# Optimization experiments

Measured on AMD Instinct MI355X. Metric: run time of the kernel, lower is better.

The kernel has to match this reference:

```python
import jax, jax.numpy as jnp
import numpy as np
import math

DIM = 2048
N_HEADS = 16
HEAD_DIM = DIM // N_HEADS
BASE = 10000
B, S = 2, 2048


def rope_cache(seq_len, head_dim, base):
    theta = 1.0 / (base ** (jnp.arange(0, head_dim, 2, dtype=jnp.float32)[: head_dim // 2] / head_dim))
    idx_theta = jnp.arange(seq_len, dtype=jnp.float32)[:, None] * theta[None, :]  # [S, D/2]
    return jnp.cos(idx_theta), jnp.sin(idx_theta)


def apply_rope(x, cos, sin):
    # x: [B, S, H, D]; cos/sin: [S, D/2]; interleaved-pair rotation
    b, s, h, d = x.shape
    xr = x.astype(jnp.float32).reshape(b, s, h, d // 2, 2)
    c = cos[None, :, None, :]
    sn = sin[None, :, None, :]
    x0, x1 = xr[..., 0], xr[..., 1]
    out = jnp.stack([x0 * c - x1 * sn, x1 * c + x0 * sn], axis=-1)
    return out.reshape(b, s, h, d).astype(x.dtype)


def setup_inputs() -> dict:
    key = jax.random.key(0)
    k1, k2, k3, k4, k5 = jax.random.split(key, 5)
    x = jax.random.normal(k1, (B, S, DIM), dtype=jnp.float32)
    # causal mask: True = masked out (strict upper triangle)
    mask = jnp.triu(jnp.ones((S, S), dtype=bool), k=1)[None, None]  # [1,1,S,S]
    scale = 0.02
    wq = jax.random.normal(k2, (DIM, DIM), dtype=jnp.float32) * scale
    wk = jax.random.normal(k3, (DIM, DIM), dtype=jnp.float32) * scale
    wv = jax.random.normal(k4, (DIM, DIM), dtype=jnp.float32) * scale
    wo = jax.random.normal(k5, (DIM, DIM), dtype=jnp.float32) * scale
    return {"x": x, "mask": mask, "wq": wq, "wk": wk, "wv": wv, "wo": wo}


def reference(x, mask, wq, wk, wv, wo):
    b, s, _ = x.shape
    cos, sin = rope_cache(s, HEAD_DIM, BASE)
    q = (x @ wq.T).reshape(b, s, N_HEADS, HEAD_DIM)
    k = (x @ wk.T).reshape(b, s, N_HEADS, HEAD_DIM)
    v = (x @ wv.T).reshape(b, s, N_HEADS, HEAD_DIM)
    q = apply_rope(q, cos, sin)
    k = apply_rope(k, cos, sin)
    # [B, H, S, S]
    scores = jnp.einsum('bqhd,bkhd->bhqk', q, k) / math.sqrt(HEAD_DIM)
    scores = jnp.where(mask, -jnp.inf, scores)
    attn = jax.nn.softmax(scores.astype(jnp.float32), axis=-1).astype(q.dtype)
    out = jnp.einsum('bhqk,bkhd->bqhd', attn, v).reshape(b, s, DIM)
    return out @ wo.T
```

## Files before the change

### kernel.cpp

```cpp
#include <hip/hip_runtime.h>
#include <hip/hip_bf16.h>
#include <math.h>

#define DIM   2048
#define NH    16
#define HD    128
#define SEQ   2048
#define BATCH 2
#define QKVN  6144

typedef __attribute__((ext_vector_type(8))) short short8;
typedef __attribute__((ext_vector_type(4))) float f32x4;
typedef __attribute__((ext_vector_type(4))) unsigned int u32x4;

static __device__ __forceinline__ unsigned short f2bf(float f) {
    __hip_bfloat16 h = __float2bfloat16(f);
    return *reinterpret_cast<unsigned short*>(&h);
}

static __device__ __forceinline__ void gload16(const __hip_bfloat16* g, __hip_bfloat16* l) {
    __builtin_amdgcn_global_load_lds(
        (__attribute__((address_space(1))) void*)(g),
        (__attribute__((address_space(3))) void*)(l), 16, 0, 0);
}

__global__ void cast_kernel(const float* __restrict__ in, __hip_bfloat16* __restrict__ out, int n) {
    int i = (blockIdx.x * blockDim.x + threadIdx.x) * 4;
    if (i >= n) return;
    float4 v = *(const float4*)(in + i);
    union { unsigned short u[4]; uint2 d; } pk;
    pk.u[0] = f2bf(v.x); pk.u[1] = f2bf(v.y); pk.u[2] = f2bf(v.z); pk.u[3] = f2bf(v.w);
    *(uint2*)(out + i) = pk.d;
}

__global__ void rope_kernel(__hip_bfloat16* __restrict__ qkv) {
    int idx = blockIdx.x * blockDim.x + threadIdx.x;
    int m    = idx >> 10;
    int rest = idx & 1023;
    int h    = rest >> 6;
    int i    = rest & 63;
    int s    = m & (SEQ - 1);
    float theta = __expf(-((float)(2 * i) * (1.0f / (float)HD)) * 9.210340371976184f);
    float ang = (float)s * theta;
    float sn, cs;
    sincosf(ang, &sn, &cs);
    size_t base = (size_t)m * QKVN + h * HD + 2 * i;
    float q0 = __bfloat162float(qkv[base]);
    float q1 = __bfloat162float(qkv[base + 1]);
    qkv[base]     = __float2bfloat16(q0 * cs - q1 * sn);
    qkv[base + 1] = __float2bfloat16(q1 * cs + q0 * sn);
    float k0 = __bfloat162float(qkv[base + DIM]);
    float k1 = __bfloat162float(qkv[base + DIM + 1]);
    qkv[base + DIM]     = __float2bfloat16(k0 * cs - k1 * sn);
    qkv[base + DIM + 1] = __float2bfloat16(k1 * cs + k0 * sn);
}

__global__ __launch_bounds__(256) void vtrans_kernel(const __hip_bfloat16* __restrict__ qkv,
                                                     __hip_bfloat16* __restrict__ vt) {
    __shared__ __align__(16) __hip_bfloat16 T[64 * 64];
    int tid = threadIdx.x;
    int s0 = blockIdx.x * 64;
    int d0 = blockIdx.y * 64;
    int b  = blockIdx.z;
#pragma unroll
    for (int i = 0; i < 2; i++) {
        int ch = tid + 256 * i;
        int r  = ch >> 3;
        int cc = ch & 7;
        u32x4 v = *(const u32x4*)(qkv + ((size_t)(b * SEQ + s0 + r)) * QKVN + 2 * DIM + d0 + cc * 8);
        __hip_bfloat16 tmp[8];
        *(u32x4*)tmp = v;
#pragma unroll
        for (int j = 0; j < 8; j++) {
            int dl = cc * 8 + j;
            int chunk = ((r >> 3) ^ (dl & 7) ^ (dl >> 3)) & 7;
            T[dl * 64 + chunk * 8 + (r & 7)] = tmp[j];
        }
    }
    __syncthreads();
#pragma unroll
    for (int i = 0; i < 2; i++) {
        int ch = tid + 256 * i;
        int dl = ch >> 3;
        int sc = ch & 7;
        int chunk = (sc ^ (dl & 7) ^ (dl >> 3)) & 7;
        u32x4 v = *(const u32x4*)(T + dl * 64 + chunk * 8);
        int d = d0 + dl;
        int h = d >> 7, dd = d & 127;
        *(u32x4*)(vt + ((size_t)((b * NH + h) * HD + dd)) * SEQ + s0 + sc * 8) = v;
    }
}

__device__ __forceinline__ void storeC(float* C, size_t idx, float v) { C[idx] = v; }
__device__ __forceinline__ void storeC(__hip_bfloat16* C, size_t idx, float v) { C[idx] = __float2bfloat16(v); }

template <typename OutT>
__global__ __launch_bounds__(256) void gemm_bt(const __hip_bfloat16* __restrict__ A,
                                               const __hip_bfloat16* __restrict__ B,
                                               OutT* __restrict__ C, int M, int N, int K) {
    constexpr int BK = 64;
    __shared__ __align__(16) __hip_bfloat16 As[128 * BK];
    __shared__ __align__(16) __hip_bfloat16 Bs[128 * BK];
    int tid  = threadIdx.x;
    int lane = tid & 63;
    int wave = tid >> 6;
    int quad = lane >> 4;
    int l15  = lane & 15;
    int wr   = wave >> 1, wc = wave & 1;
    int m0 = blockIdx.y * 128;
    int n0 = blockIdx.x * 128;
    f32x4 acc[4][4] = {};

    for (int k0 = 0; k0 < K; k0 += BK) {
        __syncthreads();
#pragma unroll
        for (int c = 0; c < 4; c++) {
            int br = (wave * 4 + c) * 8;
            int r  = br + (lane >> 3);
            int cc = (lane & 7) ^ (r & 7);
            gload16(A + (size_t)(m0 + r) * K + k0 + cc * 8, As + br * 64);
            gload16(B + (size_t)(n0 + r) * K + k0 + cc * 8, Bs + br * 64);
        }
        __syncthreads();
#pragma unroll
        for (int kk = 0; kk < BK; kk += 32) {
            short8 af[4], bf4[4];
#pragma unroll
            for (int t = 0; t < 4; t++) {
                int Ra = wr * 64 + t * 16 + l15;
                int pa = ((kk >> 3) + quad) ^ (Ra & 7);
                af[t] = *(const short8*)(As + Ra * 64 + pa * 8);
                int Rb = wc * 64 + t * 16 + l15;
                int pb = ((kk >> 3) + quad) ^ (Rb & 7);
                bf4[t] = *(const short8*)(Bs + Rb * 64 + pb * 8);
            }
#pragma unroll
            for (int mt = 0; mt < 4; mt++)
#pragma unroll
                for (int nt = 0; nt < 4; nt++)
                    acc[mt][nt] = __builtin_amdgcn_mfma_f32_16x16x32_bf16(af[mt], bf4[nt], acc[mt][nt], 0, 0, 0);
        }
    }
#pragma unroll
    for (int mt = 0; mt < 4; mt++)
#pragma unroll
        for (int nt = 0; nt < 4; nt++)
#pragma unroll
            for (int r = 0; r < 4; r++) {
                int row = m0 + wr * 64 + mt * 16 + quad * 4 + r;
                int col = n0 + wc * 64 + nt * 16 + l15;
                storeC(C, (size_t)row * N + col, acc[mt][nt][r]);
            }
}

__global__ __launch_bounds__(256) void flash_kernel(const __hip_bfloat16* __restrict__ qkv,
                                                    const __hip_bfloat16* __restrict__ vt,
                                                    __hip_bfloat16* __restrict__ attn) {
    __shared__ __align__(16) __hip_bfloat16 Ks[64 * 128];
    __shared__ __align__(16) __hip_bfloat16 Vts[128 * 64];
    constexpr int LDP = 72;
    __shared__ __align__(16) __hip_bfloat16 Ps[4 * 16 * LDP];
    int tid  = threadIdx.x;
    int lane = tid & 63;
    int wave = tid >> 6;
    int quad = lane >> 4;
    int l15  = lane & 15;
    int pairi = blockIdx.x;
    int bh = blockIdx.y;
    int b  = bh >> 4;
    int h  = bh & 15;
    size_t row0 = (size_t)b * SEQ;
    const __hip_bfloat16* vbase = vt + (size_t)bh * HD * SEQ;
    const float scale = 0.08838834764831845f;

    for (int seg = 0; seg < 2; seg++) {
        int qt = seg ? (31 - pairi) : pairi;
        short8 qf[4];
        {
            int qrow = qt * 64 + wave * 16 + l15;
            const __hip_bfloat16* qptr = qkv + (row0 + qrow) * (size_t)QKVN + h * HD + quad * 8;
#pragma unroll
            for (int c = 0; c < 4; c++) qf[c] = *(const short8*)(qptr + c * 32);
        }
        f32x4 o[8] = {};
        float mprev[4] = {-INFINITY, -INFINITY, -INFINITY, -INFINITY};
        float lsum[4]  = {0.f, 0.f, 0.f, 0.f};

        for (int kt = 0; kt <= qt; kt++) {
            __syncthreads();
#pragma unroll
            for (int c = 0; c < 4; c++) {
                int br = (wave * 4 + c) * 4;
                int r  = br + (lane >> 4);
                int cc = (lane & 15) ^ (r & 15);
                gload16(qkv + (row0 + kt * 64 + r) * (size_t)QKVN + DIM + h * HD + cc * 8,
                        Ks + br * 128);
            }
#pragma unroll
            for (int c = 0; c < 4; c++) {
                int br = (wave * 4 + c) * 8;
                int r  = br + (lane >> 3);
                int cc = (lane & 7) ^ (r & 7);
                gload16(vbase + (size_t)r * SEQ + kt * 64 + cc * 8, Vts + br * 64);
            }
            __syncthreads();

            f32x4 s[4];
#pragma unroll
            for (int nt = 0; nt < 4; nt++) {
                f32x4 a = {};
                int R = nt * 16 + l15;
#pragma unroll
                for (int c = 0; c < 4; c++) {
                    int phys = (c * 4 + quad) ^ (R & 15);
                    short8 kf = *(const short8*)(Ks + R * 128 + phys * 8);
                    a = __builtin_amdgcn_mfma_f32_16x16x32_bf16(qf[c], kf, a, 0, 0, 0);
                }
                s[nt] = a;
            }
            bool diag = (kt == qt);
#pragma unroll
            for (int nt = 0; nt < 4; nt++) {
                int key = kt * 64 + nt * 16 + l15;
#pragma unroll
                for (int r = 0; r < 4; r++) {
                    float v = s[nt][r] * scale;
                    if (diag) {
                        int q = qt * 64 + wave * 16 + quad * 4 + r;
                        if (key > q) v = -INFINITY;
                    }
                    s[nt][r] = v;
                }
            }
            float alpha[4];
#pragma unroll
            for (int r = 0; r < 4; r++) {
                float v = fmaxf(fmaxf(s[0][r], s[1][r]), fmaxf(s[2][r], s[3][r]));
                v = fmaxf(v, __shfl_xor(v, 1));
                v = fmaxf(v, __shfl_xor(v, 2));
                v = fmaxf(v, __shfl_xor(v, 4));
                v = fmaxf(v, __shfl_xor(v, 8));
                float mnew = fmaxf(mprev[r], v);
                alpha[r] = __expf(mprev[r] - mnew);
                mprev[r] = mnew;
            }
#pragma unroll
            for (int r = 0; r < 4; r++) {
                float sum = 0.f;
#pragma unroll
                for (int nt = 0; nt < 4; nt++) {
                    float p = __expf(s[nt][r] - mprev[r]);
                    s[nt][r] = p;
                    sum += p;
                }
                sum += __shfl_xor(sum, 1);
                sum += __shfl_xor(sum, 2);
                sum += __shfl_xor(sum, 4);
                sum += __shfl_xor(sum, 8);
                lsum[r] = lsum[r] * alpha[r] + sum;
            }
            __hip_bfloat16* pw = Ps + wave * 16 * LDP;
#pragma unroll
            for (int nt = 0; nt < 4; nt++)
#pragma unroll
                for (int r = 0; r < 4; r++)
                    pw[(quad * 4 + r) * LDP + nt * 16 + l15] = __float2bfloat16(s[nt][r]);
#pragma unroll
            for (int dt = 0; dt < 8; dt++)
#pragma unroll
                for (int r = 0; r < 4; r++) o[dt][r] *= alpha[r];
            short8 pf0 = *(const short8*)(pw + l15 * LDP + quad * 8);
            short8 pf1 = *(const short8*)(pw + l15 * LDP + 32 + quad * 8);
#pragma unroll
            for (int dt = 0; dt < 8; dt++) {
                int d = dt * 16 + l15;
                int p0 = (0 + quad) ^ (d & 7);
                int p1 = (4 + quad) ^ (d & 7);
                short8 vf0 = *(const short8*)(Vts + d * 64 + p0 * 8);
                short8 vf1 = *(const short8*)(Vts + d * 64 + p1 * 8);
                o[dt] = __builtin_amdgcn_mfma_f32_16x16x32_bf16(pf0, vf0, o[dt], 0, 0, 0);
                o[dt] = __builtin_amdgcn_mfma_f32_16x16x32_bf16(pf1, vf1, o[dt], 0, 0, 0);
            }
        }
        int qbase = qt * 64 + wave * 16 + quad * 4;
#pragma unroll
        for (int r = 0; r < 4; r++) {
            float inv = 1.0f / lsum[r];
#pragma unroll
            for (int dt = 0; dt < 8; dt++) {
                attn[(row0 + qbase + r) * (size_t)DIM + h * HD + dt * 16 + l15] =
                    __float2bfloat16(o[dt][r] * inv);
            }
        }
    }
}

extern "C" void kernel_launch(void* const* d_in, const int* in_sizes, int n_in,
                              void* d_out, int out_size, void* d_ws, size_t ws_size,
                              hipStream_t stream) {
    const float* x  = (const float*)d_in[0];
    const float* wq = (const float*)d_in[2];
    const float* wk = (const float*)d_in[3];
    const float* wv = (const float*)d_in[4];
    const float* wo = (const float*)d_in[5];
    float* out = (float*)d_out;

    char* ws = (char*)d_ws;
    __hip_bfloat16* xb    = (__hip_bfloat16*)(ws);
    __hip_bfloat16* attn  = (__hip_bfloat16*)(ws);
    __hip_bfloat16* wqkvb = (__hip_bfloat16*)(ws + 16777216ull);
    __hip_bfloat16* wob   = (__hip_bfloat16*)(ws + 41943040ull);
    __hip_bfloat16* qkv   = (__hip_bfloat16*)(ws + 50331648ull);
    __hip_bfloat16* vtg   = (__hip_bfloat16*)(ws + 100663296ull);

    const int nx = BATCH * SEQ * DIM;
    const int nw = DIM * DIM;
    cast_kernel<<<nx / 4 / 256, 256, 0, stream>>>(x, xb, nx);
    cast_kernel<<<nw / 4 / 256, 256, 0, stream>>>(wq, wqkvb, nw);
    cast_kernel<<<nw / 4 / 256, 256, 0, stream>>>(wk, wqkvb + (size_t)DIM * DIM, nw);
    cast_kernel<<<nw / 4 / 256, 256, 0, stream>>>(wv, wqkvb + 2ull * DIM * DIM, nw);
    cast_kernel<<<nw / 4 / 256, 256, 0, stream>>>(wo, wob, nw);

    gemm_bt<__hip_bfloat16><<<dim3(QKVN / 128, (BATCH * SEQ) / 128), 256, 0, stream>>>(
        xb, wqkvb, qkv, BATCH * SEQ, QKVN, DIM);

    rope_kernel<<<(BATCH * SEQ * NH * (HD / 2)) / 256, 256, 0, stream>>>(qkv);

    vtrans_kernel<<<dim3(SEQ / 64, DIM / 64, BATCH), 256, 0, stream>>>(qkv, vtg);

    flash_kernel<<<dim3(16, BATCH * NH), 256, 0, stream>>>(qkv, vtg, attn);

    gemm_bt<float><<<dim3(DIM / 128, (BATCH * SEQ) / 128), 256, 0, stream>>>(
        attn, wob, out, BATCH * SEQ, DIM, DIM);
}
```

Baseline: 433.3 us.

## Fuse cast launches, vectorize RoPE, and widen flash query tile to 128 rows

The five cast launches become one kernel that picks its source by index. RoPE now handles eight elements per thread with 16-byte loads and stores and uses the fast sincos. The flash kernel drops the paired query-tile scheme and gives each block one 128-row query tile, two 16-row MFMA tiles per wave, so each loaded K/V tile feeds twice as many MFMAs. The trade-off is lost causal load balancing, since blocks are still 16 per head but now cover very different amounts of work, plus higher register pressure from doubled accumulators.

```diff
diff --git a/kernel.cpp b/kernel.cpp
--- a/kernel.cpp
+++ b/kernel.cpp
@@ -24,35 +24,56 @@
         (__attribute__((address_space(3))) void*)(l), 16, 0, 0);
 }
 
-__global__ void cast_kernel(const float* __restrict__ in, __hip_bfloat16* __restrict__ out, int n) {
-    int i = (blockIdx.x * blockDim.x + threadIdx.x) * 4;
-    if (i >= n) return;
-    float4 v = *(const float4*)(in + i);
+__global__ __launch_bounds__(256) void cast_all(const float* __restrict__ x,
+                                                const float* __restrict__ wq,
+                                                const float* __restrict__ wk,
+                                                const float* __restrict__ wv,
+                                                const float* __restrict__ wo,
+                                                __hip_bfloat16* __restrict__ xb,
+                                                __hip_bfloat16* __restrict__ wqkvb,
+                                                __hip_bfloat16* __restrict__ wob) {
+    const int VX = (BATCH * SEQ * DIM) / 4;
+    const int VW = (DIM * DIM) / 4;
+    int v = blockIdx.x * blockDim.x + threadIdx.x;
+    const float* src; __hip_bfloat16* dst; int off;
+    if (v < VX)               { src = x;  dst = xb;                            off = v; }
+    else if (v < VX + VW)     { src = wq; dst = wqkvb;                         off = v - VX; }
+    else if (v < VX + 2 * VW) { src = wk; dst = wqkvb + (size_t)DIM * DIM;     off = v - VX - VW; }
+    else if (v < VX + 3 * VW) { src = wv; dst = wqkvb + 2ull * DIM * DIM;      off = v - VX - 2 * VW; }
+    else                      { src = wo; dst = wob;                           off = v - VX - 3 * VW; }
+    float4 f = *(const float4*)(src + (size_t)off * 4);
     union { unsigned short u[4]; uint2 d; } pk;
-    pk.u[0] = f2bf(v.x); pk.u[1] = f2bf(v.y); pk.u[2] = f2bf(v.z); pk.u[3] = f2bf(v.w);
-    *(uint2*)(out + i) = pk.d;
-}
-
-__global__ void rope_kernel(__hip_bfloat16* __restrict__ qkv) {
+    pk.u[0] = f2bf(f.x); pk.u[1] = f2bf(f.y); pk.u[2] = f2bf(f.z); pk.u[3] = f2bf(f.w);
+    *(uint2*)(dst + (size_t)off * 4) = pk.d;
+}
+
+__global__ __launch_bounds__(256) void rope_kernel(__hip_bfloat16* __restrict__ qkv) {
     int idx = blockIdx.x * blockDim.x + threadIdx.x;
-    int m    = idx >> 10;
-    int rest = idx & 1023;
-    int h    = rest >> 6;
-    int i    = rest & 63;
+    int m    = idx >> 8;
+    int rest = idx & 255;
+    int h    = rest >> 4;
+    int g    = rest & 15;
     int s    = m & (SEQ - 1);
-    float theta = __expf(-((float)(2 * i) * (1.0f / (float)HD)) * 9.210340371976184f);
-    float ang = (float)s * theta;
-    float sn, cs;
-    sincosf(ang, &sn, &cs);
-    size_t base = (size_t)m * QKVN + h * HD + 2 * i;
-    float q0 = __bfloat162float(qkv[base]);
-    float q1 = __bfloat162float(qkv[base + 1]);
-    qkv[base]     = __float2bfloat16(q0 * cs - q1 * sn);
-    qkv[base + 1] = __float2bfloat16(q1 * cs + q0 * sn);
-    float k0 = __bfloat162float(qkv[base + DIM]);
-    float k1 = __bfloat162float(qkv[base + DIM + 1]);
-    qkv[base + DIM]     = __float2bfloat16(k0 * cs - k1 * sn);
-    qkv[base + DIM + 1] = __float2bfloat16(k1 * cs + k0 * sn);
+    size_t base = (size_t)m * QKVN + h * HD + g * 8;
+    u32x4 qv = *(const u32x4*)(qkv + base);
+    u32x4 kv = *(const u32x4*)(qkv + base + DIM);
+    __hip_bfloat16 qa[8], ka[8];
+    *(u32x4*)qa = qv; *(u32x4*)ka = kv;
+#pragma unroll
+    for (int j = 0; j < 4; j++) {
+        int i = g * 4 + j;
+        float theta = __expf(-((float)(2 * i) * (1.0f / (float)HD)) * 9.210340371976184f);
+        float sn, cs;
+        __sincosf((float)s * theta, &sn, &cs);
+        float q0 = __bfloat162float(qa[2 * j]), q1 = __bfloat162float(qa[2 * j + 1]);
+        qa[2 * j]     = __float2bfloat16(q0 * cs - q1 * sn);
+        qa[2 * j + 1] = __float2bfloat16(q1 * cs + q0 * sn);
+        float k0 = __bfloat162float(ka[2 * j]), k1 = __bfloat162float(ka[2 * j + 1]);
+        ka[2 * j]     = __float2bfloat16(k0 * cs - k1 * sn);
+        ka[2 * j + 1] = __float2bfloat16(k1 * cs + k0 * sn);
+    }
+    *(u32x4*)(qkv + base) = *(const u32x4*)qa;
+    *(u32x4*)(qkv + base + DIM) = *(const u32x4*)ka;
 }
 
 __global__ __launch_bounds__(256) void vtrans_kernel(const __hip_bfloat16* __restrict__ qkv,
@@ -158,14 +179,14 @@
                                                     __hip_bfloat16* __restrict__ attn) {
     __shared__ __align__(16) __hip_bfloat16 Ks[64 * 128];
     __shared__ __align__(16) __hip_bfloat16 Vts[128 * 64];
-    constexpr int LDP = 72;
-    __shared__ __align__(16) __hip_bfloat16 Ps[4 * 16 * LDP];
+    constexpr int LDP = 80;
+    __shared__ __align__(16) __hip_bfloat16 Ps[4 * 32 * LDP];
     int tid  = threadIdx.x;
     int lane = tid & 63;
     int wave = tid >> 6;
     int quad = lane >> 4;
     int l15  = lane & 15;
-    int pairi = blockIdx.x;
+    int qt = 15 - blockIdx.x;
     int bh = blockIdx.y;
     int b  = bh >> 4;
     int h  = bh & 15;
@@ -173,123 +194,135 @@
     const __hip_bfloat16* vbase = vt + (size_t)bh * HD * SEQ;
     const float scale = 0.08838834764831845f;
 
-    for (int seg = 0; seg < 2; seg++) {
-        int qt = seg ? (31 - pairi) : pairi;
-        short8 qf[4];
-        {
-            int qrow = qt * 64 + wave * 16 + l15;
-            const __hip_bfloat16* qptr = qkv + (row0 + qrow) * (size_t)QKVN + h * HD + quad * 8;
-#pragma unroll
-            for (int c = 0; c < 4; c++) qf[c] = *(const short8*)(qptr + c * 32);
-        }
-        f32x4 o[8] = {};
-        float mprev[4] = {-INFINITY, -INFINITY, -INFINITY, -INFINITY};
-        float lsum[4]  = {0.f, 0.f, 0.f, 0.f};
-
-        for (int kt = 0; kt <= qt; kt++) {
-            __syncthreads();
+    short8 qf[2][4];
+#pragma unroll
+    for (int mt = 0; mt < 2; mt++) {
+        int qrow = qt * 128 + wave * 32 + mt * 16 + l15;
+        const __hip_bfloat16* qptr = qkv + (row0 + qrow) * (size_t)QKVN + h * HD + quad * 8;
+#pragma unroll
+        for (int c = 0; c < 4; c++) qf[mt][c] = *(const short8*)(qptr + c * 32);
+    }
+    f32x4 o[2][8] = {};
+    float mprev[2][4], lsum[2][4];
+#pragma unroll
+    for (int mt = 0; mt < 2; mt++)
+#pragma unroll
+        for (int r = 0; r < 4; r++) { mprev[mt][r] = -INFINITY; lsum[mt][r] = 0.f; }
+
+    int ktend = 2 * qt + 2;
+    for (int kt = 0; kt < ktend; kt++) {
+        __syncthreads();
+#pragma unroll
+        for (int c = 0; c < 4; c++) {
+            int br = (wave * 4 + c) * 4;
+            int r  = br + (lane >> 4);
+            int cc = (lane & 15) ^ (r & 15);
+            gload16(qkv + (row0 + kt * 64 + r) * (size_t)QKVN + DIM + h * HD + cc * 8,
+                    Ks + br * 128);
+        }
+#pragma unroll
+        for (int c = 0; c < 4; c++) {
+            int br = (wave * 4 + c) * 8;
+            int r  = br + (lane >> 3);
+            int cc = (lane & 7) ^ (r & 7);
+            gload16(vbase + (size_t)r * SEQ + kt * 64 + cc * 8, Vts + br * 64);
+        }
+        __syncthreads();
+
+        f32x4 s[2][4];
+#pragma unroll
+        for (int nt = 0; nt < 4; nt++) {
+            f32x4 a0 = {}, a1 = {};
+            int R = nt * 16 + l15;
 #pragma unroll
             for (int c = 0; c < 4; c++) {
-                int br = (wave * 4 + c) * 4;
-                int r  = br + (lane >> 4);
-                int cc = (lane & 15) ^ (r & 15);
-                gload16(qkv + (row0 + kt * 64 + r) * (size_t)QKVN + DIM + h * HD + cc * 8,
-                        Ks + br * 128);
-            }
-#pragma unroll
-            for (int c = 0; c < 4; c++) {
-                int br = (wave * 4 + c) * 8;
-                int r  = br + (lane >> 3);
-                int cc = (lane & 7) ^ (r & 7);
-                gload16(vbase + (size_t)r * SEQ + kt * 64 + cc * 8, Vts + br * 64);
-            }
-            __syncthreads();
-
-            f32x4 s[4];
-#pragma unroll
-            for (int nt = 0; nt < 4; nt++) {
-                f32x4 a = {};
-                int R = nt * 16 + l15;
-#pragma unroll
-                for (int c = 0; c < 4; c++) {
-                    int phys = (c * 4 + quad) ^ (R & 15);
-                    short8 kf = *(const short8*)(Ks + R * 128 + phys * 8);
-                    a = __builtin_amdgcn_mfma_f32_16x16x32_bf16(qf[c], kf, a, 0, 0, 0);
-                }
-                s[nt] = a;
-            }
-            bool diag = (kt == qt);
+                int phys = (c * 4 + quad) ^ (R & 15);
+                short8 kf = *(const short8*)(Ks + R * 128 + phys * 8);
+                a0 = __builtin_amdgcn_mfma_f32_16x16x32_bf16(qf[0][c], kf, a0, 0, 0, 0);
+                a1 = __builtin_amdgcn_mfma_f32_16x16x32_bf16(qf[1][c], kf, a1, 0, 0, 0);
+            }
+            s[0][nt] = a0; s[1][nt] = a1;
+        }
+        bool diag = (kt >= 2 * qt);
+#pragma unroll
+        for (int mt = 0; mt < 2; mt++) {
 #pragma unroll
             for (int nt = 0; nt < 4; nt++) {
                 int key = kt * 64 + nt * 16 + l15;
 #pragma unroll
                 for (int r = 0; r < 4; r++) {
-                    float v = s[nt][r] * scale;
+                    float v = s[mt][nt][r] * scale;
                     if (diag) {
-                        int q = qt * 64 + wave * 16 + quad * 4 + r;
+                        int q = qt * 128 + wave * 32 + mt * 16 + quad * 4 + r;
                         if (key > q) v = -INFINITY;
                     }
-                    s[nt][r] = v;
+                    s[mt][nt][r] = v;
                 }
             }
-            float alpha[4];
 #pragma unroll
             for (int r = 0; r < 4; r++) {
-                float v = fmaxf(fmaxf(s[0][r], s[1][r]), fmaxf(s[2][r], s[3][r]));
+                float v = fmaxf(fmaxf(s[mt][0][r], s[mt][1][r]), fmaxf(s[mt][2][r], s[mt][3][r]));
                 v = fmaxf(v, __shfl_xor(v, 1));
                 v = fmaxf(v, __shfl_xor(v, 2));
                 v = fmaxf(v, __shfl_xor(v, 4));
                 v = fmaxf(v, __shfl_xor(v, 8));
-                float mnew = fmaxf(mprev[r], v);
-                alpha[r] = __expf(mprev[r] - mnew);
-                mprev[r] = mnew;
-            }
-#pragma unroll
-            for (int r = 0; r < 4; r++) {
+                float mnew = fmaxf(mprev[mt][r], v);
+                float alpha = __expf(mprev[mt][r] - mnew);
+                mprev[mt][r] = mnew;
                 float sum = 0.f;
 #pragma unroll
                 for (int nt = 0; nt < 4; nt++) {
-                    float p = __expf(s[nt][r] - mprev[r]);
-                    s[nt][r] = p;
+                    float p = __expf(s[mt][nt][r] - mnew);
+                    s[mt][nt][r] = p;
                     sum += p;
                 }
                 sum += __shfl_xor(sum, 1);
                 sum += __shfl_xor(sum, 2);
                 sum += __shfl_xor(sum, 4);
                 sum += __shfl_xor(sum, 8);
-                lsum[r] = lsum[r] * alpha[r] + sum;
-            }
-            __hip_bfloat16* pw = Ps + wave * 16 * LDP;
+                lsum[mt][r] = lsum[mt][r] * alpha + sum;
+#pragma unroll
+                for (int dt = 0; dt < 8; dt++) o[mt][dt][r] *= alpha;
+            }
+        }
+        __hip_bfloat16* pw = Ps + wave * 32 * LDP;
+#pragma unroll
+        for (int mt = 0; mt < 2; mt++)
 #pragma unroll
             for (int nt = 0; nt < 4; nt++)
 #pragma unroll
                 for (int r = 0; r < 4; r++)
-                    pw[(quad * 4 + r) * LDP + nt * 16 + l15] = __float2bfloat16(s[nt][r]);
-#pragma unroll
-            for (int dt = 0; dt < 8; dt++)
-#pragma unroll
-                for (int r = 0; r < 4; r++) o[dt][r] *= alpha[r];
-            short8 pf0 = *(const short8*)(pw + l15 * LDP + quad * 8);
-            short8 pf1 = *(const short8*)(pw + l15 * LDP + 32 + quad * 8);
-#pragma unroll
-            for (int dt = 0; dt < 8; dt++) {
-                int d = dt * 16 + l15;
-                int p0 = (0 + quad) ^ (d & 7);
-                int p1 = (4 + quad) ^ (d & 7);
-                short8 vf0 = *(const short8*)(Vts + d * 64 + p0 * 8);
-                short8 vf1 = *(const short8*)(Vts + d * 64 + p1 * 8);
-                o[dt] = __builtin_amdgcn_mfma_f32_16x16x32_bf16(pf0, vf0, o[dt], 0, 0, 0);
-                o[dt] = __builtin_amdgcn_mfma_f32_16x16x32_bf16(pf1, vf1, o[dt], 0, 0, 0);
-            }
-        }
-        int qbase = qt * 64 + wave * 16 + quad * 4;
+                    pw[(mt * 16 + quad * 4 + r) * LDP + nt * 16 + l15] = __float2bfloat16(s[mt][nt][r]);
+        short8 pf[2][2];
+#pragma unroll
+        for (int mt = 0; mt < 2; mt++) {
+            pf[mt][0] = *(const short8*)(pw + (mt * 16 + l15) * LDP + quad * 8);
+            pf[mt][1] = *(const short8*)(pw + (mt * 16 + l15) * LDP + 32 + quad * 8);
+        }
+#pragma unroll
+        for (int dt = 0; dt < 8; dt++) {
+            int d = dt * 16 + l15;
+            int p0 = (0 + quad) ^ (d & 7);
+            int p1 = (4 + quad) ^ (d & 7);
+            short8 vf0 = *(const short8*)(Vts + d * 64 + p0 * 8);
+            short8 vf1 = *(const short8*)(Vts + d * 64 + p1 * 8);
+#pragma unroll
+            for (int mt = 0; mt < 2; mt++) {
+                o[mt][dt] = __builtin_amdgcn_mfma_f32_16x16x32_bf16(pf[mt][0], vf0, o[mt][dt], 0, 0, 0);
+                o[mt][dt] = __builtin_amdgcn_mfma_f32_16x16x32_bf16(pf[mt][1], vf1, o[mt][dt], 0, 0, 0);
+            }
+        }
+    }
+#pragma unroll
+    for (int mt = 0; mt < 2; mt++) {
+        int qbase = qt * 128 + wave * 32 + mt * 16 + quad * 4;
 #pragma unroll
         for (int r = 0; r < 4; r++) {
-            float inv = 1.0f / lsum[r];
+            float inv = 1.0f / lsum[mt][r];
 #pragma unroll
             for (int dt = 0; dt < 8; dt++) {
                 attn[(row0 + qbase + r) * (size_t)DIM + h * HD + dt * 16 + l15] =
-                    __float2bfloat16(o[dt][r] * inv);
+                    __float2bfloat16(o[mt][dt][r] * inv);
             }
         }
     }
@@ -313,18 +346,13 @@
     __hip_bfloat16* qkv   = (__hip_bfloat16*)(ws + 50331648ull);
     __hip_bfloat16* vtg   = (__hip_bfloat16*)(ws + 100663296ull);
 
-    const int nx = BATCH * SEQ * DIM;
-    const int nw = DIM * DIM;
-    cast_kernel<<<nx / 4 / 256, 256, 0, stream>>>(x, xb, nx);
-    cast_kernel<<<nw / 4 / 256, 256, 0, stream>>>(wq, wqkvb, nw);
-    cast_kernel<<<nw / 4 / 256, 256, 0, stream>>>(wk, wqkvb + (size_t)DIM * DIM, nw);
-    cast_kernel<<<nw / 4 / 256, 256, 0, stream>>>(wv, wqkvb + 2ull * DIM * DIM, nw);
-    cast_kernel<<<nw / 4 / 256, 256, 0, stream>>>(wo, wob, nw);
+    const int nv = (BATCH * SEQ * DIM + 4 * DIM * DIM) / 4;
+    cast_all<<<nv / 256, 256, 0, stream>>>(x, wq, wk, wv, wo, xb, wqkvb, wob);
 
     gemm_bt<__hip_bfloat16><<<dim3(QKVN / 128, (BATCH * SEQ) / 128), 256, 0, stream>>>(
         xb, wqkvb, qkv, BATCH * SEQ, QKVN, DIM);
 
-    rope_kernel<<<(BATCH * SEQ * NH * (HD / 2)) / 256, 256, 0, stream>>>(qkv);
+    rope_kernel<<<(BATCH * SEQ * NH * 16) / 256, 256, 0, stream>>>(qkv);
 
     vtrans_kernel<<<dim3(SEQ / 64, DIM / 64, BATCH), 256, 0, stream>>>(qkv, vtg);
 
```

After: 534.8 us. 23.4% more time.
